# Optimization experiments

Measured on AMD Instinct MI355X. Metric: run time of the kernel, lower is better.

The kernel has to match this reference:

```python
import jax, jax.numpy as jnp
import numpy as np

BIG = 1e10  # sentinel for masked-out (padded) points, like pytorch3d's masking


def setup_inputs() -> dict:
    key = jax.random.key(0)
    k1, k2, k3, k4 = jax.random.split(key, 4)
    B, N, M = 16, 4096, 4096
    source_cloud = jax.random.normal(k1, (B, N, 2), dtype=jnp.float32)
    target_cloud = jax.random.normal(k2, (B, M, 2), dtype=jnp.float32)
    source_mask = jax.random.randint(k3, (B,), 0, N)  # lengths1
    target_mask = jax.random.randint(k4, (B,), 0, M)  # lengths2
    return {
        "source_cloud": source_cloud,
        "target_cloud": target_cloud,
        "source_mask": source_mask,
        "target_mask": target_mask,
    }


def reference(source_cloud, target_cloud, source_mask, target_mask):
    # source_cloud: [B, N, 2], target_cloud: [B, M, 2]
    # source_mask/target_mask: int lengths [B] (knn_points lengths1/lengths2)
    B, N, _ = source_cloud.shape
    M = target_cloud.shape[1]

    s2 = jnp.sum(source_cloud * source_cloud, axis=-1)  # [B, N]
    t2 = jnp.sum(target_cloud * target_cloud, axis=-1)  # [B, M]
    # squared pairwise distances [B, N, M]
    d2 = (s2[:, :, None] + t2[:, None, :]
          - 2.0 * jnp.einsum('bnd,bmd->bnm', source_cloud, target_cloud))

    src_valid = jnp.arange(N)[None, :] < source_mask[:, None]  # [B, N]
    tgt_valid = jnp.arange(M)[None, :] < target_mask[:, None]  # [B, M]

    # forward: for each source point, 1-NN over valid target points
    d2_fwd = jnp.where(tgt_valid[:, None, :], d2, BIG)
    min_fwd = jnp.maximum(jnp.min(d2_fwd, axis=-1), 0.0)  # [B, N]
    # backward: for each target point, 1-NN over valid source points
    d2_bwd = jnp.where(src_valid[:, :, None], d2, BIG)
    min_bwd = jnp.maximum(jnp.min(d2_bwd, axis=-2), 0.0)  # [B, M]

    # padded query points get dist 0 (pytorch3d knn_points semantics), then sqrt
    chamfer_forward = jnp.where(src_valid, jnp.sqrt(min_fwd), 0.0)
    chamfer_backward = jnp.where(tgt_valid, jnp.sqrt(min_bwd), 0.0)
    return (chamfer_forward, chamfer_backward)
```

## Files before the change

### kernel.cpp

```cpp
#include <hip/hip_runtime.h>


#define NQ 16

__global__ __launch_bounds__(256, 2) void chamfer_main(
    const float* __restrict__ src, const float* __restrict__ tgt,
    const int* __restrict__ slen, const int* __restrict__ tlen,
    unsigned int* __restrict__ out_bits)
{
    __shared__ float4 sh[256];

    const int bx  = blockIdx.x;
    const int dir = bx >> 8;
    const int b   = (bx >> 4) & 15;
    const int pc  = bx & 15;
    const int tid = threadIdx.x;

    const float* Q = dir ? tgt : src;
    const float* P = dir ? src : tgt;
    const int Lp = dir ? slen[b] : tlen[b];

    {
        const float2 p = ((const float2*)P)[b * 4096 + pc * 256 + tid];
        sh[tid] = make_float4(p.x, p.y, fmaf(p.x, p.x, p.y * p.y), 0.f);
    }
    __syncthreads();

    int count = Lp - pc * 256;
    count = count < 0 ? 0 : (count > 256 ? 256 : count);
    if (count == 0) return;

    float m2x[NQ], m2y[NQ], s2[NQ], best[NQ];
    #pragma unroll
    for (int k = 0; k < NQ; ++k) {
        const float2 q = ((const float2*)Q)[b * 4096 + tid + k * 256];
        m2x[k] = -2.f * q.x;
        m2y[k] = -2.f * q.y;
        s2[k]  = fmaf(q.x, q.x, q.y * q.y);
        best[k] = 3.0e38f;
    }

    #pragma unroll 4
    for (int j = 0; j < count; ++j) {
        const float4 t = sh[j];
        #pragma unroll
        for (int k = 0; k < NQ; ++k) {
            float v = fmaf(m2x[k], t.x, t.z);
            v = fmaf(m2y[k], t.y, v);
            best[k] = fminf(best[k], v);
        }
    }

    unsigned int* row = out_bits + dir * 65536 + b * 4096;
    #pragma unroll
    for (int k = 0; k < NQ; ++k) {
        const float d2 = fmaxf(best[k] + s2[k], 0.f);
        atomicMin(&row[tid + k * 256], __float_as_uint(d2));
    }
}

__global__ __launch_bounds__(256) void chamfer_epilogue(
    unsigned int* __restrict__ out_bits,
    const int* __restrict__ slen, const int* __restrict__ tlen)
{
    const int idx = blockIdx.x * 256 + threadIdx.x;
    const int dir = idx >> 16;
    const int b   = (idx >> 12) & 15;
    const int i   = idx & 4095;
    const int L   = dir ? tlen[b] : slen[b];
    float r = 0.f;
    if (i < L) {
        const unsigned int bits = out_bits[idx];
        r = (bits == 0xFFFFFFFFu) ? 100000.0f
                                  : sqrtf(__uint_as_float(bits));
    }
    ((float*)out_bits)[idx] = r;
}

extern "C" void kernel_launch(void* const* d_in, const int* in_sizes, int n_in,
                              void* d_out, int out_size, void* d_ws, size_t ws_size,
                              hipStream_t stream) {
    const float* src = (const float*)d_in[0];
    const float* tgt = (const float*)d_in[1];
    const int* slen  = (const int*)d_in[2];
    const int* tlen  = (const int*)d_in[3];
    unsigned int* out_bits = (unsigned int*)d_out;

    hipMemsetAsync(out_bits, 0xFF, (size_t)131072 * 4, stream);
    chamfer_main<<<512, 256, 0, stream>>>(src, tgt, slen, tlen, out_bits);
    chamfer_epilogue<<<512, 256, 0, stream>>>(out_bits, slen, tlen);
}
```

Before: 90.83 us.

## Fuse chamfer into single kernel with per-thread full scan and packed FMA

Replaces the memset, the atomicMin main kernel and the epilogue with one kernel in which each 64-thread block owns 128 query points of one batch row and scans every valid reference point. Each thread holds two queries and processes reference points in pairs with packed float2 FMA, reading them directly from global memory rather than LDS. This removes two launches, the atomics and the output round trip. In exchange each thread carries a long serial loop, with 1024 small blocks and no shared-memory reuse, which risks lower occupancy and longer latency per block. Empty target sets now give sqrt(1e10) instead of 1e5.

```diff
diff --git a/kernel.cpp b/kernel.cpp
--- a/kernel.cpp
+++ b/kernel.cpp
@@ -1,80 +1,58 @@
 #include <hip/hip_runtime.h>
 
 
-#define NQ 16
+typedef float f2 __attribute__((ext_vector_type(2)));
 
-__global__ __launch_bounds__(256, 2) void chamfer_main(
+__global__ __launch_bounds__(64) void chamfer_fused(
     const float* __restrict__ src, const float* __restrict__ tgt,
     const int* __restrict__ slen, const int* __restrict__ tlen,
-    unsigned int* __restrict__ out_bits)
+    float* __restrict__ out)
 {
-    __shared__ float4 sh[256];
-
-    const int bx  = blockIdx.x;
-    const int dir = bx >> 8;
-    const int b   = (bx >> 4) & 15;
-    const int pc  = bx & 15;
-    const int tid = threadIdx.x;
+    const int blk  = blockIdx.x;
+    const int row  = blk >> 5;
+    const int qc   = blk & 31;
+    const int dir  = row >> 4, b = row & 15;
+    const int lane = threadIdx.x;
 
     const float* Q = dir ? tgt : src;
     const float* P = dir ? src : tgt;
+    const int Lq = dir ? tlen[b] : slen[b];
     const int Lp = dir ? slen[b] : tlen[b];
 
-    {
-        const float2 p = ((const float2*)P)[b * 4096 + pc * 256 + tid];
-        sh[tid] = make_float4(p.x, p.y, fmaf(p.x, p.x, p.y * p.y), 0.f);
-    }
-    __syncthreads();
+    const int q0 = qc * 128 + lane * 2;
+    const float4 qq = ((const float4*)(Q + (size_t)b * 8192))[q0 >> 1];
 
-    int count = Lp - pc * 256;
-    count = count < 0 ? 0 : (count > 256 ? 256 : count);
-    if (count == 0) return;
+    const f2 mx0 = f2{-2.f * qq.x, -2.f * qq.x};
+    const f2 my0 = f2{-2.f * qq.y, -2.f * qq.y};
+    const f2 mx1 = f2{-2.f * qq.z, -2.f * qq.z};
+    const f2 my1 = f2{-2.f * qq.w, -2.f * qq.w};
+    const float s20 = fmaf(qq.x, qq.x, qq.y * qq.y);
+    const float s21 = fmaf(qq.z, qq.z, qq.w * qq.w);
+    float b0 = 3.0e38f, b1 = 3.0e38f;
 
-    float m2x[NQ], m2y[NQ], s2[NQ], best[NQ];
-    #pragma unroll
-    for (int k = 0; k < NQ; ++k) {
-        const float2 q = ((const float2*)Q)[b * 4096 + tid + k * 256];
-        m2x[k] = -2.f * q.x;
-        m2y[k] = -2.f * q.y;
-        s2[k]  = fmaf(q.x, q.x, q.y * q.y);
-        best[k] = 3.0e38f;
+    const float4* pts = (const float4*)(P + (size_t)b * 8192);
+    const int nrec = (Lp + 1) >> 1;
+    #pragma unroll 4
+    for (int j = 0; j < nrec; ++j) {
+        const float4 pp = pts[j];
+        const float x1 = (2 * j + 1 < Lp) ? pp.z : 1e15f;
+        const f2 xp = f2{pp.x, x1};
+        const f2 yp = f2{pp.y, pp.w};
+        const f2 np = __builtin_elementwise_fma(xp, xp, yp * yp);
+        f2 v0 = __builtin_elementwise_fma(xp, mx0, np);
+        v0 = __builtin_elementwise_fma(yp, my0, v0);
+        b0 = fminf(b0, fminf(v0.x, v0.y));
+        f2 v1 = __builtin_elementwise_fma(xp, mx1, np);
+        v1 = __builtin_elementwise_fma(yp, my1, v1);
+        b1 = fminf(b1, fminf(v1.x, v1.y));
     }
 
-    #pragma unroll 4
-    for (int j = 0; j < count; ++j) {
-        const float4 t = sh[j];
-        #pragma unroll
-        for (int k = 0; k < NQ; ++k) {
-            float v = fmaf(m2x[k], t.x, t.z);
-            v = fmaf(m2y[k], t.y, v);
-            best[k] = fminf(best[k], v);
-        }
-    }
-
-    unsigned int* row = out_bits + dir * 65536 + b * 4096;
-    #pragma unroll
-    for (int k = 0; k < NQ; ++k) {
-        const float d2 = fmaxf(best[k] + s2[k], 0.f);
-        atomicMin(&row[tid + k * 256], __float_as_uint(d2));
-    }
-}
-
-__global__ __launch_bounds__(256) void chamfer_epilogue(
-    unsigned int* __restrict__ out_bits,
-    const int* __restrict__ slen, const int* __restrict__ tlen)
-{
-    const int idx = blockIdx.x * 256 + threadIdx.x;
-    const int dir = idx >> 16;
-    const int b   = (idx >> 12) & 15;
-    const int i   = idx & 4095;
-    const int L   = dir ? tlen[b] : slen[b];
-    float r = 0.f;
-    if (i < L) {
-        const unsigned int bits = out_bits[idx];
-        r = (bits == 0xFFFFFFFFu) ? 100000.0f
-                                  : sqrtf(__uint_as_float(bits));
-    }
-    ((float*)out_bits)[idx] = r;
+    const float d0 = (Lp > 0) ? fmaxf(b0 + s20, 0.f) : 1e10f;
+    const float d1 = (Lp > 0) ? fmaxf(b1 + s21, 0.f) : 1e10f;
+    float2 r;
+    r.x = (q0     < Lq) ? sqrtf(d0) : 0.f;
+    r.y = (q0 + 1 < Lq) ? sqrtf(d1) : 0.f;
+    ((float2*)(out + (size_t)row * 4096))[q0 >> 1] = r;
 }
 
 extern "C" void kernel_launch(void* const* d_in, const int* in_sizes, int n_in,
@@ -84,9 +62,6 @@
     const float* tgt = (const float*)d_in[1];
     const int* slen  = (const int*)d_in[2];
     const int* tlen  = (const int*)d_in[3];
-    unsigned int* out_bits = (unsigned int*)d_out;
 
-    hipMemsetAsync(out_bits, 0xFF, (size_t)131072 * 4, stream);
-    chamfer_main<<<512, 256, 0, stream>>>(src, tgt, slen, tlen, out_bits);
-    chamfer_epilogue<<<512, 256, 0, stream>>>(out_bits, slen, tlen);
+    chamfer_fused<<<1024, 64, 0, stream>>>(src, tgt, slen, tlen, (float*)d_out);
 }
```

Result: slower. 214.6 us (+136.3%).
